# Kernel tuning notes

Hardware: AMD Instinct MI355X
Metric: run time of the kernel (lower is better)

The kernel has to match this reference:

```python
import jax, jax.numpy as jnp
import numpy as np

LEAK = 0.01


def setup_inputs() -> dict:
    key = jax.random.key(0)
    k1, k2, k3, k4 = jax.random.split(key, 4)
    N, I, O, H, E = 20000, 128, 128, 4, 320000
    input_h = jax.random.normal(k1, (N, I), dtype=jnp.float32)
    edges = jax.random.randint(k2, (E, 3), 0, N, dtype=jnp.int64)
    # xavier-normal-ish scale for W (H,O,I) and a (H,1,2O)
    W = jax.random.normal(k3, (H, O, I), dtype=jnp.float32) * np.float32(np.sqrt(2.0 / (O + I)))
    a = jax.random.normal(k4, (H, 1, 2 * O), dtype=jnp.float32) * np.float32(np.sqrt(2.0 / (1 + 2 * O)))
    return {"input_h": input_h, "edges": edges, "W": W, "a": a}


def reference(input_h, edges, W, a):
    H, O, _ = W.shape
    N = input_h.shape[0]
    src, rel, dst = edges[:, 0], edges[:, 1], edges[:, 2]
    # per-head projection: x[h,n,o] = sum_i W[h,o,i] * input_h[n,i]
    x = jnp.einsum('hoi,ni->hno', W, input_h)            # (H,N,O)
    h = x.sum(axis=0) / H                                # (N,O)
    # attention scores: (cat([x_src, x_dst]) * a).sum(-1), split a to avoid the concat
    a_src = a[:, 0, :O]                                  # (H,O)
    a_dst = a[:, 0, O:]                                  # (H,O)
    x_dst = x[:, dst]                                    # (H,E,O)
    scores = jnp.einsum('heo,ho->he', x[:, src], a_src) + jnp.einsum('heo,ho->he', x_dst, a_dst)
    # NOTE: faithful to original — softmax is over ALL edges per head
    att = jax.nn.softmax(jax.nn.leaky_relu(scores, LEAK), axis=-1)  # (H,E)
    message = (x_dst * att[..., None]).reshape(-1, O)    # (H*E, O), head-major like torch.cat
    src_rep = jnp.tile(src, H)                           # (H*E,)
    agg = jax.ops.segment_sum(message, src_rep, num_segments=N)  # (N,O)
    return h + agg / H
```

## Files before the change

kernel.cpp:

```cpp
#include <hip/hip_runtime.h>

#define NF 128
#define NH 4
#define BCAP 64

typedef __attribute__((ext_vector_type(4))) float f32x4;
typedef __attribute__((ext_vector_type(8))) short bf16x8;

#define FP4C 0.7f
#define FP4INV (1.0f / FP4C)

__device__ __forceinline__ float b2f(unsigned short u) {
  return __uint_as_float(((unsigned)u) << 16);
}
__device__ __forceinline__ unsigned short f2b(float f) {
  unsigned u = __float_as_uint(f);
  unsigned r = ((u >> 16) & 1u) + 0x7fffu;
  return (unsigned short)((u + r) >> 16);
}

__global__ __launch_bounds__(256) void k_prep0(
    const float* __restrict__ W, unsigned short* __restrict__ Wfhi) {
  int i = blockIdx.x * 256 + threadIdx.x;
  int h = i >> 11, rem = i & 2047;
  int o = rem >> 4, i0 = (rem & 15) * 8;
  const float* p = W + (size_t)(h * NF + o) * NF + i0;
  float4 a = *(const float4*)p, b = *(const float4*)(p + 4);
  float vv[8] = {a.x, a.y, a.z, a.w, b.x, b.y, b.z, b.w};
  bf16x8 hi8;
  #pragma unroll
  for (int j = 0; j < 8; ++j) hi8[j] = (short)f2b(vv[j]);
  int rec = (((o >> 4) * 4 + h) * 4 + (i0 >> 5)) * 64 +
            ((i0 >> 3) & 3) * 16 + (o & 15);
  *(bf16x8*)(Wfhi + (size_t)rec * 8) = hi8;
}

__global__ __launch_bounds__(256) void k1_mfma(
    const float* __restrict__ inp, const unsigned short* __restrict__ Wfhi,
    const float* __restrict__ ag, unsigned int* __restrict__ x4,
    float* __restrict__ s4s, float* __restrict__ s4d,
    float* __restrict__ out, int* __restrict__ cnt, int N) {
  __shared__ unsigned short sAhi[8 * 64 * 8];
  __shared__ unsigned short sAlo[8 * 64 * 8];
  __shared__ unsigned short xL[4 * 8 * 2 * 64 * 4];
  const int t = threadIdx.x, w = t >> 6, l = t & 63;
  const int col = l & 15, quad = l >> 4;
  const int n0 = blockIdx.x * 32;

  if (t < 32) cnt[n0 + t] = 0;

  #pragma unroll
  for (int rho = 0; rho < 2; ++rho) {
    int slab = rho * 4 + w;
    const float* p = inp + (size_t)(n0 + rho * 16 + col) * NF + w * 32 + quad * 8;
    float4 v0 = *(const float4*)p, v1 = *(const float4*)(p + 4);
    float vv[8] = {v0.x, v0.y, v0.z, v0.w, v1.x, v1.y, v1.z, v1.w};
    bf16x8 hi8, lo8;
    #pragma unroll
    for (int j = 0; j < 8; ++j) {
      unsigned short hi = f2b(vv[j]);
      hi8[j] = (short)hi;
      lo8[j] = (short)f2b(vv[j] - b2f(hi));
    }
    *(bf16x8*)(sAhi + (slab * 64 + l) * 8) = hi8;
    *(bf16x8*)(sAlo + (slab * 64 + l) * 8) = lo8;
  }
  __syncthreads();

  bf16x8 Ah[2][4], Al[2][4];
  #pragma unroll
  for (int tau = 0; tau < 2; ++tau)
    #pragma unroll
    for (int s = 0; s < 4; ++s) {
      Ah[tau][s] = *(bf16x8*)(sAhi + ((tau * 4 + s) * 64 + l) * 8);
      Al[tau][s] = *(bf16x8*)(sAlo + ((tau * 4 + s) * 64 + l) * 8);
    }

  float as8[8], ad8[8];
  #pragma unroll
  for (int ot = 0; ot < 8; ++ot) {
    as8[ot] = ag[w * 2 * NF + ot * 16 + col];
    ad8[ot] = ag[w * 2 * NF + NF + ot * 16 + col];
  }

  const bf16x8* WH = (const bf16x8*)Wfhi;
  bf16x8 cur[4];
  #pragma unroll
  for (int s = 0; s < 4; ++s) cur[s] = WH[(size_t)((0 * 4 + w) * 4 + s) * 64 + l];

  float ps[2][4] = {{0.f}}, pd[2][4] = {{0.f}};
  #pragma unroll
  for (int ot = 0; ot < 8; ++ot) {
    bf16x8 nxt[4];
    if (ot < 7) {
      #pragma unroll
      for (int s = 0; s < 4; ++s)
        nxt[s] = WH[(size_t)(((ot + 1) * 4 + w) * 4 + s) * 64 + l];
    }
    #pragma unroll
    for (int tau = 0; tau < 2; ++tau) {
      f32x4 acc = {0.f, 0.f, 0.f, 0.f};
      #pragma unroll
      for (int s = 0; s < 4; ++s) {
        acc = __builtin_amdgcn_mfma_f32_16x16x32_bf16(Al[tau][s], cur[s], acc, 0, 0, 0);
        acc = __builtin_amdgcn_mfma_f32_16x16x32_bf16(Ah[tau][s], cur[s], acc, 0, 0, 0);
      }
      ushort4 xs;
      #pragma unroll
      for (int r = 0; r < 4; ++r) {
        ps[tau][r] = fmaf(acc[r], as8[ot], ps[tau][r]);
        pd[tau][r] = fmaf(acc[r], ad8[ot], pd[tau][r]);
      }
      xs.x = f2b(acc[0]); xs.y = f2b(acc[1]);
      xs.z = f2b(acc[2]); xs.w = f2b(acc[3]);
      *(ushort4*)(xL + (((w * 8 + ot) * 2 + tau) * 64 + l) * 4) = xs;
    }
    if (ot < 7) {
      #pragma unroll
      for (int s = 0; s < 4; ++s) cur[s] = nxt[s];
    }
  }

  #pragma unroll
  for (int m = 1; m < 16; m <<= 1)
    #pragma unroll
    for (int tau = 0; tau < 2; ++tau)
      #pragma unroll
      for (int r = 0; r < 4; ++r) {
        ps[tau][r] += __shfl_xor(ps[tau][r], m);
        pd[tau][r] += __shfl_xor(pd[tau][r], m);
      }
  if (col == 0) {
    #pragma unroll
    for (int tau = 0; tau < 2; ++tau)
      #pragma unroll
      for (int r = 0; r < 4; ++r) {
        int n = n0 + tau * 16 + quad * 4 + r;
        s4s[n * 4 + w] = ps[tau][r];
        s4d[n * 4 + w] = pd[tau][r];
      }
  }
  __syncthreads();

  {
    int c2 = t & 7, qd = (t >> 3) & 3, tau = (t >> 5) & 1, otg = t >> 6;
    #pragma unroll
    for (int io = 0; io < 2; ++io) {
      int ot = otg * 2 + io;
      float xv[4][4][2];
      #pragma unroll
      for (int h = 0; h < NH; ++h) {
        int slab = (h * 8 + ot) * 2 + tau;
        ushort4 qa = *(const ushort4*)(xL + (slab * 64 + qd * 16 + c2 * 2) * 4);
        ushort4 qb = *(const ushort4*)(xL + (slab * 64 + qd * 16 + c2 * 2 + 1) * 4);
        xv[h][0][0] = b2f(qa.x); xv[h][1][0] = b2f(qa.y);
        xv[h][2][0] = b2f(qa.z); xv[h][3][0] = b2f(qa.w);
        xv[h][0][1] = b2f(qb.x); xv[h][1][1] = b2f(qb.y);
        xv[h][2][1] = b2f(qb.z); xv[h][3][1] = b2f(qb.w);
      }
      #pragma unroll
      for (int r = 0; r < 4; ++r) {
        int n = n0 + tau * 16 + qd * 4 + r;
        float o0 = 0.25f * (xv[0][r][0] + xv[1][r][0] + xv[2][r][0] + xv[3][r][0]);
        float o1 = 0.25f * (xv[0][r][1] + xv[1][r][1] + xv[2][r][1] + xv[3][r][1]);
        *(float2*)(out + (size_t)n * NF + ot * 16 + c2 * 2) = make_float2(o0, o1);
        unsigned q = 0;
        #pragma unroll
        for (int h = 0; h < NH; ++h) {
          int q0 = __float2int_rn(xv[h][r][0] * FP4INV + 7.5f);
          int q1 = __float2int_rn(xv[h][r][1] * FP4INV + 7.5f);
          q0 = q0 < 0 ? 0 : (q0 > 15 ? 15 : q0);
          q1 = q1 < 0 ? 0 : (q1 > 15 ? 15 : q1);
          q |= ((unsigned)q0) << (4 * h);
          q |= ((unsigned)q1) << (4 * (4 + h));
        }
        x4[(size_t)n * 64 + ot * 8 + c2] = q;
      }
    }
  }
}

__global__ __launch_bounds__(256) void k_edge(
    const int* __restrict__ edges, const float4* __restrict__ s4s,
    const float4* __restrict__ s4d, int* __restrict__ cnt,
    uint4* __restrict__ recs, float4* __restrict__ Zpart, int N, int E) {
  int base = (blockIdx.x * 256 + threadIdx.x) * 2;
  float z0 = 0.f, z1 = 0.f, z2 = 0.f, z3 = 0.f;
  #pragma unroll
  for (int k = 0; k < 2; ++k) {
    int e = base + k;
    if (e < E) {
      int s = edges[3 * (size_t)e];
      int d = edges[3 * (size_t)e + 2];
      float4 ss = s4s[s];
      float4 dd = s4d[d];
      float sc[4] = {ss.x + dd.x, ss.y + dd.y, ss.z + dd.z, ss.w + dd.w};
      float v[4];
      #pragma unroll
      for (int h = 0; h < NH; ++h) {
        float u = sc[h] > 0.f ? sc[h] : 0.01f * sc[h];
        v[h] = __expf(u);
      }
      z0 += v[0]; z1 += v[1]; z2 += v[2]; z3 += v[3];
      unsigned evx = (unsigned)f2b(v[0]) | ((unsigned)f2b(v[1]) << 16);
      unsigned evy = (unsigned)f2b(v[2]) | ((unsigned)f2b(v[3]) << 16);
      int rk = atomicAdd(&cnt[s], 1);
      if (rk < BCAP)
        recs[(size_t)s * BCAP + rk] = make_uint4((unsigned)d, evx, evy, 0u);
    }
  }
  #pragma unroll
  for (int m = 32; m; m >>= 1) {
    z0 += __shfl_xor(z0, m, 64);
    z1 += __shfl_xor(z1, m, 64);
    z2 += __shfl_xor(z2, m, 64);
    z3 += __shfl_xor(z3, m, 64);
  }
  if ((threadIdx.x & 63) == 0)
    Zpart[blockIdx.x * 4 + (threadIdx.x >> 6)] = make_float4(z0, z1, z2, z3);
}

__global__ __launch_bounds__(256) void k_sumz(
    const float* __restrict__ Zpart, int nw, float* __restrict__ invZ) {
  int w = threadIdx.x >> 6, lane = threadIdx.x & 63;
  float s = 0.f;
  for (int i = lane; i < nw; i += 64) s += Zpart[i * 4 + w];
  #pragma unroll
  for (int m = 32; m; m >>= 1) s += __shfl_xor(s, m, 64);
  if (lane == 0) invZ[w] = 0.25f / s;
}

__global__ __launch_bounds__(256) void k_agg(
    const uint4* __restrict__ recs, const int* __restrict__ cnt,
    const float* __restrict__ invZ, const unsigned int* __restrict__ x4,
    float* __restrict__ out, int N) {
  __shared__ uint4 rsh[4][BCAP];
  int wv = threadIdx.x >> 6;
  int n = (int)((blockIdx.x * 256 + threadIdx.x) >> 6);
  int lane = threadIdx.x & 63;
  if (n >= N) return;
  int deg = cnt[n];
  if (deg == 0) return;
  if (deg > BCAP) deg = BCAP;
  if (lane < deg) rsh[wv][lane] = recs[(size_t)n * BCAP + lane];
  float A00 = 0.f, A01 = 0.f, A10 = 0.f, A11 = 0.f;
  float A20 = 0.f, A21 = 0.f, A30 = 0.f, A31 = 0.f;
  float S0 = 0.f, S1 = 0.f, S2 = 0.f, S3 = 0.f;
  for (int i = 0; i < deg; ++i) {
    uint4 rec = rsh[wv][i];
    unsigned q = x4[(size_t)rec.x * 64 + lane];
    float w0 = b2f((unsigned short)(rec.y & 0xffffu));
    float w1 = b2f((unsigned short)(rec.y >> 16));
    float w2 = b2f((unsigned short)(rec.z & 0xffffu));
    float w3 = b2f((unsigned short)(rec.z >> 16));
    S0 += w0; S1 += w1; S2 += w2; S3 += w3;
    A00 = fmaf(w0, (float)(q & 15u), A00);
    A10 = fmaf(w1, (float)((q >> 4) & 15u), A10);
    A20 = fmaf(w2, (float)((q >> 8) & 15u), A20);
    A30 = fmaf(w3, (float)((q >> 12) & 15u), A30);
    A01 = fmaf(w0, (float)((q >> 16) & 15u), A01);
    A11 = fmaf(w1, (float)((q >> 20) & 15u), A11);
    A21 = fmaf(w2, (float)((q >> 24) & 15u), A21);
    A31 = fmaf(w3, (float)(q >> 28), A31);
  }
  float z0 = invZ[0], z1 = invZ[1], z2 = invZ[2], z3 = invZ[3];
  float t0 = z0 * A00 + z1 * A10 + z2 * A20 + z3 * A30;
  float t1 = z0 * A01 + z1 * A11 + z2 * A21 + z3 * A31;
  float sz = z0 * S0 + z1 * S1 + z2 * S2 + z3 * S3;
  float r0 = FP4C * t0 - 7.5f * FP4C * sz;
  float r1 = FP4C * t1 - 7.5f * FP4C * sz;
  float2* op = (float2*)(out + (size_t)n * NF + lane * 2);
  float2 cur = *op;
  cur.x += r0;
  cur.y += r1;
  *op = cur;
}

extern "C" void kernel_launch(void* const* d_in, const int* in_sizes, int n_in,
                              void* d_out, int out_size, void* d_ws, size_t ws_size,
                              hipStream_t stream) {
  const float* inp   = (const float*)d_in[0];
  const int*   edges = (const int*)d_in[1];
  const float* Wg    = (const float*)d_in[2];
  const float* ag    = (const float*)d_in[3];
  float*       out   = (float*)d_out;
  const int N = in_sizes[0] / NF;
  const int E = in_sizes[1] / 3;
  const int nblkE = (E + 511) / 512;
  const int nw = nblkE * 4;

  char* ws = (char*)d_ws;
  size_t off = 0;
  unsigned int* x4 = (unsigned int*)(ws + off); off += (size_t)N * 64 * 4;
  float* s4s = (float*)(ws + off); off += (size_t)N * 4 * 4;
  float* s4d = (float*)(ws + off); off += (size_t)N * 4 * 4;
  uint4* recs = (uint4*)(ws + off); off += (size_t)N * BCAP * 16;
  unsigned short* Wfhi = (unsigned short*)(ws + off); off += (size_t)NH * NF * NF * 2;
  int* cnt = (int*)(ws + off); off += (size_t)N * 4;
  float* invZ = (float*)(ws + off); off += 16;
  float* Zpart = (float*)(ws + off); off += (size_t)nw * 16;

  k_prep0<<<32, 256, 0, stream>>>(Wg, Wfhi);
  k1_mfma<<<N / 32, 256, 0, stream>>>(inp, Wfhi, ag, x4, s4s, s4d, out, cnt, N);
  k_edge<<<nblkE, 256, 0, stream>>>(edges, (const float4*)s4s,
                                    (const float4*)s4d, cnt, recs,
                                    (float4*)Zpart, N, E);
  k_sumz<<<1, 256, 0, stream>>>(Zpart, nw, invZ);
  k_agg<<<(N * 64 + 255) / 256, 256, 0, stream>>>(recs, cnt, invZ, x4, out, N);
}
```

Measured before the change: 138.8 us.

## Fuse edge scoring, softmax normalizer and aggregation into one kernel with grid barrier

Merges the edge-scoring kernel, the normalizer-reduction kernel and the aggregation kernel into a single persistent launch. Blocks first write per-block partial sums, then meet at a spin-wait barrier on an atomic arrival counter, reduce the normalizer redundantly in every block, and each block then aggregates 16 nodes. Zeroing of the degree counters moves into the weight-prep kernel, which is enlarged to cover N. This removes two kernel launches and their inter-kernel gaps, but it depends on all 1250 blocks being co-resident (launch bounds of 5 blocks per CU), or the barrier deadlocks. It also adds spin-wait and fence overhead.

```diff
diff --git a/kernel.cpp b/kernel.cpp
--- a/kernel.cpp
+++ b/kernel.cpp
@@ -20,34 +20,37 @@
 }
 
 __global__ __launch_bounds__(256) void k_prep0(
-    const float* __restrict__ W, unsigned short* __restrict__ Wfhi) {
+    const float* __restrict__ W, unsigned short* __restrict__ Wfhi,
+    int* __restrict__ cnt, int* __restrict__ arrive, int N) {
   int i = blockIdx.x * 256 + threadIdx.x;
-  int h = i >> 11, rem = i & 2047;
-  int o = rem >> 4, i0 = (rem & 15) * 8;
-  const float* p = W + (size_t)(h * NF + o) * NF + i0;
-  float4 a = *(const float4*)p, b = *(const float4*)(p + 4);
-  float vv[8] = {a.x, a.y, a.z, a.w, b.x, b.y, b.z, b.w};
-  bf16x8 hi8;
-  #pragma unroll
-  for (int j = 0; j < 8; ++j) hi8[j] = (short)f2b(vv[j]);
-  int rec = (((o >> 4) * 4 + h) * 4 + (i0 >> 5)) * 64 +
-            ((i0 >> 3) & 3) * 16 + (o & 15);
-  *(bf16x8*)(Wfhi + (size_t)rec * 8) = hi8;
+  if (i < 8192) {
+    int h = i >> 11, rem = i & 2047;
+    int o = rem >> 4, i0 = (rem & 15) * 8;
+    const float* p = W + (size_t)(h * NF + o) * NF + i0;
+    float4 a = *(const float4*)p, b = *(const float4*)(p + 4);
+    float vv[8] = {a.x, a.y, a.z, a.w, b.x, b.y, b.z, b.w};
+    bf16x8 hi8;
+    #pragma unroll
+    for (int j = 0; j < 8; ++j) hi8[j] = (short)f2b(vv[j]);
+    int rec = (((o >> 4) * 4 + h) * 4 + (i0 >> 5)) * 64 +
+              ((i0 >> 3) & 3) * 16 + (o & 15);
+    *(bf16x8*)(Wfhi + (size_t)rec * 8) = hi8;
+  }
+  if (i < N) cnt[i] = 0;
+  if (i == 0) *arrive = 0;
 }
 
 __global__ __launch_bounds__(256) void k1_mfma(
     const float* __restrict__ inp, const unsigned short* __restrict__ Wfhi,
     const float* __restrict__ ag, unsigned int* __restrict__ x4,
     float* __restrict__ s4s, float* __restrict__ s4d,
-    float* __restrict__ out, int* __restrict__ cnt, int N) {
+    float* __restrict__ out, int N) {
   __shared__ unsigned short sAhi[8 * 64 * 8];
   __shared__ unsigned short sAlo[8 * 64 * 8];
   __shared__ unsigned short xL[4 * 8 * 2 * 64 * 4];
   const int t = threadIdx.x, w = t >> 6, l = t & 63;
   const int col = l & 15, quad = l >> 4;
   const int n0 = blockIdx.x * 32;
-
-  if (t < 32) cnt[n0 + t] = 0;
 
   #pragma unroll
   for (int rho = 0; rho < 2; ++rho) {
@@ -180,34 +183,65 @@
   }
 }
 
-__global__ __launch_bounds__(256) void k_edge(
+__global__ __launch_bounds__(256, 5) void k_edge_agg(
     const int* __restrict__ edges, const float4* __restrict__ s4s,
     const float4* __restrict__ s4d, int* __restrict__ cnt,
-    uint4* __restrict__ recs, float4* __restrict__ Zpart, int N, int E) {
-  int base = (blockIdx.x * 256 + threadIdx.x) * 2;
+    uint4* __restrict__ recs, const unsigned int* __restrict__ x4,
+    float4* __restrict__ Zpart, int* __restrict__ arrive,
+    float* __restrict__ out, int N, int E, int nblk) {
+  __shared__ uint4 rsh[4][BCAP];
+  __shared__ float4 zsh[4];
+  __shared__ float4 zld[4];
+  const int t = threadIdx.x, wv = t >> 6, lane = t & 63;
+  const int b = blockIdx.x;
+
+  float v0 = 0.f, v1 = 0.f, v2 = 0.f, v3 = 0.f;
+  int e = b * 256 + t;
+  if (e < E) {
+    int s = edges[3 * (size_t)e];
+    int d = edges[3 * (size_t)e + 2];
+    float4 ss = s4s[s];
+    float4 dd = s4d[d];
+    float sc0 = ss.x + dd.x, sc1 = ss.y + dd.y;
+    float sc2 = ss.z + dd.z, sc3 = ss.w + dd.w;
+    v0 = __expf(sc0 > 0.f ? sc0 : 0.01f * sc0);
+    v1 = __expf(sc1 > 0.f ? sc1 : 0.01f * sc1);
+    v2 = __expf(sc2 > 0.f ? sc2 : 0.01f * sc2);
+    v3 = __expf(sc3 > 0.f ? sc3 : 0.01f * sc3);
+    unsigned evx = (unsigned)f2b(v0) | ((unsigned)f2b(v1) << 16);
+    unsigned evy = (unsigned)f2b(v2) | ((unsigned)f2b(v3) << 16);
+    int rk = atomicAdd(&cnt[s], 1);
+    if (rk < BCAP)
+      recs[(size_t)s * BCAP + rk] = make_uint4((unsigned)d, evx, evy, 0u);
+  }
+  #pragma unroll
+  for (int m = 32; m; m >>= 1) {
+    v0 += __shfl_xor(v0, m, 64);
+    v1 += __shfl_xor(v1, m, 64);
+    v2 += __shfl_xor(v2, m, 64);
+    v3 += __shfl_xor(v3, m, 64);
+  }
+  if (lane == 0) zsh[wv] = make_float4(v0, v1, v2, v3);
+  __syncthreads();
+
+  if (t == 0) {
+    float4 a0 = zsh[0], a1 = zsh[1], a2 = zsh[2], a3 = zsh[3];
+    Zpart[b] = make_float4(a0.x + a1.x + a2.x + a3.x, a0.y + a1.y + a2.y + a3.y,
+                           a0.z + a1.z + a2.z + a3.z, a0.w + a1.w + a2.w + a3.w);
+    __threadfence();
+    atomicAdd(arrive, 1);
+    while (__hip_atomic_load(arrive, __ATOMIC_ACQUIRE,
+                             __HIP_MEMORY_SCOPE_AGENT) < nblk) {
+      __builtin_amdgcn_s_sleep(8);
+    }
+  }
+  __syncthreads();
+  __threadfence();
+
   float z0 = 0.f, z1 = 0.f, z2 = 0.f, z3 = 0.f;
-  #pragma unroll
-  for (int k = 0; k < 2; ++k) {
-    int e = base + k;
-    if (e < E) {
-      int s = edges[3 * (size_t)e];
-      int d = edges[3 * (size_t)e + 2];
-      float4 ss = s4s[s];
-      float4 dd = s4d[d];
-      float sc[4] = {ss.x + dd.x, ss.y + dd.y, ss.z + dd.z, ss.w + dd.w};
-      float v[4];
-      #pragma unroll
-      for (int h = 0; h < NH; ++h) {
-        float u = sc[h] > 0.f ? sc[h] : 0.01f * sc[h];
-        v[h] = __expf(u);
-      }
-      z0 += v[0]; z1 += v[1]; z2 += v[2]; z3 += v[3];
-      unsigned evx = (unsigned)f2b(v[0]) | ((unsigned)f2b(v[1]) << 16);
-      unsigned evy = (unsigned)f2b(v[2]) | ((unsigned)f2b(v[3]) << 16);
-      int rk = atomicAdd(&cnt[s], 1);
-      if (rk < BCAP)
-        recs[(size_t)s * BCAP + rk] = make_uint4((unsigned)d, evx, evy, 0u);
-    }
+  for (int i = t; i < nblk; i += 256) {
+    float4 z = Zpart[i];
+    z0 += z.x; z1 += z.y; z2 += z.z; z3 += z.w;
   }
   #pragma unroll
   for (int m = 32; m; m >>= 1) {
@@ -216,64 +250,57 @@
     z2 += __shfl_xor(z2, m, 64);
     z3 += __shfl_xor(z3, m, 64);
   }
-  if ((threadIdx.x & 63) == 0)
-    Zpart[blockIdx.x * 4 + (threadIdx.x >> 6)] = make_float4(z0, z1, z2, z3);
-}
-
-__global__ __launch_bounds__(256) void k_sumz(
-    const float* __restrict__ Zpart, int nw, float* __restrict__ invZ) {
-  int w = threadIdx.x >> 6, lane = threadIdx.x & 63;
-  float s = 0.f;
-  for (int i = lane; i < nw; i += 64) s += Zpart[i * 4 + w];
-  #pragma unroll
-  for (int m = 32; m; m >>= 1) s += __shfl_xor(s, m, 64);
-  if (lane == 0) invZ[w] = 0.25f / s;
-}
-
-__global__ __launch_bounds__(256) void k_agg(
-    const uint4* __restrict__ recs, const int* __restrict__ cnt,
-    const float* __restrict__ invZ, const unsigned int* __restrict__ x4,
-    float* __restrict__ out, int N) {
-  __shared__ uint4 rsh[4][BCAP];
-  int wv = threadIdx.x >> 6;
-  int n = (int)((blockIdx.x * 256 + threadIdx.x) >> 6);
-  int lane = threadIdx.x & 63;
-  if (n >= N) return;
-  int deg = cnt[n];
-  if (deg == 0) return;
-  if (deg > BCAP) deg = BCAP;
-  if (lane < deg) rsh[wv][lane] = recs[(size_t)n * BCAP + lane];
-  float A00 = 0.f, A01 = 0.f, A10 = 0.f, A11 = 0.f;
-  float A20 = 0.f, A21 = 0.f, A30 = 0.f, A31 = 0.f;
-  float S0 = 0.f, S1 = 0.f, S2 = 0.f, S3 = 0.f;
-  for (int i = 0; i < deg; ++i) {
-    uint4 rec = rsh[wv][i];
-    unsigned q = x4[(size_t)rec.x * 64 + lane];
-    float w0 = b2f((unsigned short)(rec.y & 0xffffu));
-    float w1 = b2f((unsigned short)(rec.y >> 16));
-    float w2 = b2f((unsigned short)(rec.z & 0xffffu));
-    float w3 = b2f((unsigned short)(rec.z >> 16));
-    S0 += w0; S1 += w1; S2 += w2; S3 += w3;
-    A00 = fmaf(w0, (float)(q & 15u), A00);
-    A10 = fmaf(w1, (float)((q >> 4) & 15u), A10);
-    A20 = fmaf(w2, (float)((q >> 8) & 15u), A20);
-    A30 = fmaf(w3, (float)((q >> 12) & 15u), A30);
-    A01 = fmaf(w0, (float)((q >> 16) & 15u), A01);
-    A11 = fmaf(w1, (float)((q >> 20) & 15u), A11);
-    A21 = fmaf(w2, (float)((q >> 24) & 15u), A21);
-    A31 = fmaf(w3, (float)(q >> 28), A31);
-  }
-  float z0 = invZ[0], z1 = invZ[1], z2 = invZ[2], z3 = invZ[3];
-  float t0 = z0 * A00 + z1 * A10 + z2 * A20 + z3 * A30;
-  float t1 = z0 * A01 + z1 * A11 + z2 * A21 + z3 * A31;
-  float sz = z0 * S0 + z1 * S1 + z2 * S2 + z3 * S3;
-  float r0 = FP4C * t0 - 7.5f * FP4C * sz;
-  float r1 = FP4C * t1 - 7.5f * FP4C * sz;
-  float2* op = (float2*)(out + (size_t)n * NF + lane * 2);
-  float2 cur = *op;
-  cur.x += r0;
-  cur.y += r1;
-  *op = cur;
+  if (lane == 0) zld[wv] = make_float4(z0, z1, z2, z3);
+  __syncthreads();
+  {
+    float4 a0 = zld[0], a1 = zld[1], a2 = zld[2], a3 = zld[3];
+    z0 = 0.25f / (a0.x + a1.x + a2.x + a3.x);
+    z1 = 0.25f / (a0.y + a1.y + a2.y + a3.y);
+    z2 = 0.25f / (a0.z + a1.z + a2.z + a3.z);
+    z3 = 0.25f / (a0.w + a1.w + a2.w + a3.w);
+  }
+
+  #pragma unroll 1
+  for (int j = 0; j < 4; ++j) {
+    int n = b * 16 + wv * 4 + j;
+    if (n >= N) break;
+    int deg;
+    if (lane == 0) deg = atomicAdd(&cnt[n], 0);
+    deg = __shfl(deg, 0, 64);
+    if (deg == 0) continue;
+    if (deg > BCAP) deg = BCAP;
+    if (lane < deg) rsh[wv][lane] = recs[(size_t)n * BCAP + lane];
+    float A00 = 0.f, A01 = 0.f, A10 = 0.f, A11 = 0.f;
+    float A20 = 0.f, A21 = 0.f, A30 = 0.f, A31 = 0.f;
+    float S0 = 0.f, S1 = 0.f, S2 = 0.f, S3 = 0.f;
+    for (int i = 0; i < deg; ++i) {
+      uint4 rec = rsh[wv][i];
+      unsigned q = x4[(size_t)rec.x * 64 + lane];
+      float w0 = b2f((unsigned short)(rec.y & 0xffffu));
+      float w1 = b2f((unsigned short)(rec.y >> 16));
+      float w2 = b2f((unsigned short)(rec.z & 0xffffu));
+      float w3 = b2f((unsigned short)(rec.z >> 16));
+      S0 += w0; S1 += w1; S2 += w2; S3 += w3;
+      A00 = fmaf(w0, (float)(q & 15u), A00);
+      A10 = fmaf(w1, (float)((q >> 4) & 15u), A10);
+      A20 = fmaf(w2, (float)((q >> 8) & 15u), A20);
+      A30 = fmaf(w3, (float)((q >> 12) & 15u), A30);
+      A01 = fmaf(w0, (float)((q >> 16) & 15u), A01);
+      A11 = fmaf(w1, (float)((q >> 20) & 15u), A11);
+      A21 = fmaf(w2, (float)((q >> 24) & 15u), A21);
+      A31 = fmaf(w3, (float)(q >> 28), A31);
+    }
+    float t0 = z0 * A00 + z1 * A10 + z2 * A20 + z3 * A30;
+    float t1 = z0 * A01 + z1 * A11 + z2 * A21 + z3 * A31;
+    float sz = z0 * S0 + z1 * S1 + z2 * S2 + z3 * S3;
+    float r0 = FP4C * t0 - 7.5f * FP4C * sz;
+    float r1 = FP4C * t1 - 7.5f * FP4C * sz;
+    float2* op = (float2*)(out + (size_t)n * NF + lane * 2);
+    float2 cur = *op;
+    cur.x += r0;
+    cur.y += r1;
+    *op = cur;
+  }
 }
 
 extern "C" void kernel_launch(void* const* d_in, const int* in_sizes, int n_in,
@@ -286,8 +313,7 @@
   float*       out   = (float*)d_out;
   const int N = in_sizes[0] / NF;
   const int E = in_sizes[1] / 3;
-  const int nblkE = (E + 511) / 512;
-  const int nw = nblkE * 4;
+  const int nblk = (E + 255) / 256;
 
   char* ws = (char*)d_ws;
   size_t off = 0;
@@ -297,14 +323,12 @@
   uint4* recs = (uint4*)(ws + off); off += (size_t)N * BCAP * 16;
   unsigned short* Wfhi = (unsigned short*)(ws + off); off += (size_t)NH * NF * NF * 2;
   int* cnt = (int*)(ws + off); off += (size_t)N * 4;
-  float* invZ = (float*)(ws + off); off += 16;
-  float* Zpart = (float*)(ws + off); off += (size_t)nw * 16;
-
-  k_prep0<<<32, 256, 0, stream>>>(Wg, Wfhi);
-  k1_mfma<<<N / 32, 256, 0, stream>>>(inp, Wfhi, ag, x4, s4s, s4d, out, cnt, N);
-  k_edge<<<nblkE, 256, 0, stream>>>(edges, (const float4*)s4s,
-                                    (const float4*)s4d, cnt, recs,
-                                    (float4*)Zpart, N, E);
-  k_sumz<<<1, 256, 0, stream>>>(Zpart, nw, invZ);
-  k_agg<<<(N * 64 + 255) / 256, 256, 0, stream>>>(recs, cnt, invZ, x4, out, N);
-}
+  int* arrive = (int*)(ws + off); off += 16;
+  float4* Zpart = (float4*)(ws + off); off += (size_t)nblk * 16;
+
+  k_prep0<<<(N + 255) / 256, 256, 0, stream>>>(Wg, Wfhi, cnt, arrive, N);
+  k1_mfma<<<N / 32, 256, 0, stream>>>(inp, Wfhi, ag, x4, s4s, s4d, out, N);
+  k_edge_agg<<<nblk, 256, 0, stream>>>(edges, (const float4*)s4s,
+                                       (const float4*)s4d, cnt, recs, x4,
+                                       Zpart, arrive, out, N, E, nblk);
+}
```

New measurement: 358.6 us. 2.58x slower.
